# Optimization experiments

Hardware: AMD Instinct MI355X
Metric: run time of the kernel (lower is better)

## Reference

```python
import jax, jax.numpy as jnp
import numpy as np
import math

B, S, DIM = 1, 2048, 2048
H, KVH, HD = 32, 8, 64
REP = H // KVH


def _rope_cache(seqlen, head_dim, base=10000.0):
    # (seqlen, 2*head_dim): [cos | sin], each duplicated across both halves
    inv_freq = 1.0 / (base ** (np.arange(0, head_dim, 2, dtype=np.float32) / head_dim))
    t = np.arange(seqlen, dtype=np.float32)
    ang = np.outer(t, inv_freq)                    # (S, HD/2)
    ang = np.concatenate([ang, ang], axis=-1)      # (S, HD)
    return jnp.asarray(np.concatenate([np.cos(ang), np.sin(ang)], axis=-1))


def setup_inputs() -> dict:
    key = jax.random.key(0)
    ks = jax.random.split(key, 12)
    std = 0.02
    return {
        "x": jax.random.normal(ks[0], (B, S, DIM), jnp.float32),
        "rope_cache": _rope_cache(S, HD),
        "wq_w": jax.random.normal(ks[1], (H * HD, DIM), jnp.float32) * std,
        "wq_b": jax.random.normal(ks[2], (H * HD,), jnp.float32) * std,
        "wk_w": jax.random.normal(ks[3], (KVH * HD, DIM), jnp.float32) * std,
        "wk_b": jax.random.normal(ks[4], (KVH * HD,), jnp.float32) * std,
        "wv_w": jax.random.normal(ks[5], (KVH * HD, DIM), jnp.float32) * std,
        "wv_b": jax.random.normal(ks[6], (KVH * HD,), jnp.float32) * std,
        "wo_w": jax.random.normal(ks[7], (DIM, H * HD), jnp.float32) * std,
        "wo_b": jax.random.normal(ks[8], (DIM,), jnp.float32) * std,
        "sinks": jax.random.normal(ks[9], (H,), jnp.float32) * std,
    }


def _rotate_half(t):
    h = t.shape[-1] // 2
    return jnp.concatenate([-t[..., h:], t[..., :h]], axis=-1)


def reference(x, rope_cache, wq_w, wq_b, wk_w, wk_b, wv_w, wv_b, wo_w, wo_b, sinks):
    bsz, seqlen, _ = x.shape
    q = (jnp.einsum('bsd,od->bso', x, wq_w) + wq_b).reshape(bsz, seqlen, H, HD)
    k = (jnp.einsum('bsd,od->bso', x, wk_w) + wk_b).reshape(bsz, seqlen, KVH, HD)
    v = (jnp.einsum('bsd,od->bso', x, wv_w) + wv_b).reshape(bsz, seqlen, KVH, HD)

    cos = rope_cache[:seqlen, :HD][None, :, None, :]
    sin = rope_cache[:seqlen, HD:][None, :, None, :]
    q = q * cos + _rotate_half(q) * sin
    k = k * cos + _rotate_half(k) * sin

    # repeat_kv: repeat_interleave along head dim
    k = jnp.repeat(k, REP, axis=2)  # (B,S,H,HD)
    v = jnp.repeat(v, REP, axis=2)

    q = q.transpose(0, 2, 1, 3)  # (B,H,S,HD)
    k = k.transpose(0, 2, 1, 3)
    v = v.transpose(0, 2, 1, 3)

    scale = 1.0 / math.sqrt(HD)
    scores = jnp.einsum('bhqd,bhkd->bhqk', q, k) * scale
    causal = jnp.tril(jnp.ones((seqlen, seqlen), dtype=bool))
    scores = jnp.where(causal, scores, -jnp.inf)

    m = jnp.max(scores, axis=-1, keepdims=True)
    lse = m[..., 0] + jnp.log(jnp.sum(jnp.exp(scores - m), axis=-1))  # (B,H,S)
    attn = jnp.exp(scores - lse[..., None])
    out = jnp.einsum('bhqk,bhkd->bhqd', attn, v)

    # sink-token LSE renormalization
    combined_lse = jnp.logaddexp(lse, sinks[None, :, None])
    renorm = jnp.exp(jnp.clip(lse - combined_lse, -20.0, 0.0))
    out = out * renorm[..., None]

    out = out.transpose(0, 2, 1, 3).reshape(bsz, seqlen, H * HD)
    return jnp.einsum('bso,do->bsd', out, wo_w) + wo_b
```

## Files before the change

kernel.cpp:

```cpp
#include <hip/hip_runtime.h>


#define S_LEN 2048
#define DIM_  2048
#define QK_LD 2560

typedef __attribute__((ext_vector_type(8))) __bf16 bf16x8;
typedef __attribute__((ext_vector_type(4))) float f32x4;
typedef __attribute__((ext_vector_type(4))) unsigned short us4;

__device__ __forceinline__ unsigned short f2bf(float f) {
    union { float f; unsigned u; } v; v.f = f;
    unsigned r = v.u + 0x7FFFu + ((v.u >> 16) & 1u);
    return (unsigned short)(r >> 16);
}
__device__ __forceinline__ float bf2f(unsigned short u) {
    union { unsigned u; float f; } v; v.u = ((unsigned)u) << 16;
    return v.f;
}

__device__ __forceinline__ void gload_lds16(const void* g, void* l) {
    __builtin_amdgcn_global_load_lds(
        (const __attribute__((address_space(1))) void*)g,
        (__attribute__((address_space(3))) void*)l, 16, 0, 0);
}

__device__ __forceinline__ int swz32(int r, int ch) { return r*32 + ((ch ^ ((r >> 1) & 3)) << 3); }
__device__ __forceinline__ int swz64(int r, int ch) { return r*64 + ((ch ^ (r & 7)) << 3); }

__global__ void cvt_all(const float* __restrict__ x,  const float* __restrict__ wq,
                        const float* __restrict__ wk, const float* __restrict__ wv,
                        const float* __restrict__ wo,
                        unsigned short* __restrict__ xb,
                        unsigned short* __restrict__ wqkv,
                        unsigned short* __restrict__ wob) {
    const int i4 = blockIdx.x * 256 + threadIdx.x;
    const float* src; unsigned short* dst; int off;
    if (i4 < 1048576)      { src = x;  dst = xb;             off = i4; }
    else if (i4 < 2097152) { src = wq; dst = wqkv;           off = i4 - 1048576; }
    else if (i4 < 2359296) { src = wk; dst = wqkv + 4194304; off = i4 - 2097152; }
    else if (i4 < 2621440) { src = wv; dst = wqkv + 5242880; off = i4 - 2359296; }
    else                   { src = wo; dst = wob;            off = i4 - 2621440; }
    const float4 v = reinterpret_cast<const float4*>(src)[off];
    us4 o = { f2bf(v.x), f2bf(v.y), f2bf(v.z), f2bf(v.w) };
    reinterpret_cast<us4*>(dst)[off] = o;
}

__global__ void build_bias(const float* __restrict__ qb, const float* __restrict__ kb,
                           const float* __restrict__ vb, float* __restrict__ out) {
    const int i = blockIdx.x * 256 + threadIdx.x;
    if (i < 2048) out[i] = qb[i];
    else if (i < 2560) out[i] = kb[i - 2048];
    else if (i < 3072) out[i] = vb[i - 2560];
}

template<int MODE>
__global__ __launch_bounds__(256)
void gemm_bt(const unsigned short* __restrict__ A,
             const unsigned short* __restrict__ B,
             const float* __restrict__ bias,
             unsigned short* __restrict__ Cqk,
             unsigned short* __restrict__ Vt,
             float* __restrict__ Cf,
             int K)
{
    __shared__ unsigned short As[128 * 32];
    __shared__ unsigned short Bs[128 * 32];
    const int t = threadIdx.x;
    const int lane = t & 63;
    const int w = t >> 6;
    const int wr = w >> 1, wc = w & 1;
    const int lq = lane & 15;
    const int g = lane >> 4;
    const int m0 = blockIdx.y * 128;
    const int n0 = blockIdx.x * 128;

    const f32x4 z = {0.f, 0.f, 0.f, 0.f};
    f32x4 acc[4][4];
    #pragma unroll
    for (int i = 0; i < 4; i++)
        #pragma unroll
        for (int j = 0; j < 4; j++) acc[i][j] = z;

    for (int k0 = 0; k0 < K; k0 += 32) {
        #pragma unroll
        for (int c = 0; c < 2; c++) {
            const int chunk = w * 128 + c * 64 + lane;
            const int r = chunk >> 2;
            const int chl = (chunk & 3) ^ ((r >> 1) & 3);
            gload_lds16(&A[(size_t)(m0 + r) * K + k0 + (chl << 3)],
                        &As[(size_t)(w * 128 + c * 64) * 8]);
            gload_lds16(&B[(size_t)(n0 + r) * K + k0 + (chl << 3)],
                        &Bs[(size_t)(w * 128 + c * 64) * 8]);
        }
        __syncthreads();
        bf16x8 a[4], b[4];
        #pragma unroll
        for (int mi = 0; mi < 4; mi++)
            a[mi] = *reinterpret_cast<const bf16x8*>(&As[swz32(wr * 64 + mi * 16 + lq, g)]);
        #pragma unroll
        for (int ni = 0; ni < 4; ni++)
            b[ni] = *reinterpret_cast<const bf16x8*>(&Bs[swz32(wc * 64 + ni * 16 + lq, g)]);
        #pragma unroll
        for (int mi = 0; mi < 4; mi++)
            #pragma unroll
            for (int ni = 0; ni < 4; ni++)
                acc[mi][ni] = __builtin_amdgcn_mfma_f32_16x16x32_bf16(a[mi], b[ni], acc[mi][ni], 0, 0, 0);
        __syncthreads();
    }

    #pragma unroll
    for (int mi = 0; mi < 4; mi++) {
        const int row0 = m0 + wr * 64 + mi * 16 + g * 4;
        #pragma unroll
        for (int ni = 0; ni < 4; ni++) {
            const int col = n0 + wc * 64 + ni * 16 + lq;
            const float bv = bias[col];
            if (MODE == 1) {
                #pragma unroll
                for (int j = 0; j < 4; j++)
                    Cf[(size_t)(row0 + j) * 2048 + col] = acc[mi][ni][j] + bv;
            } else {
                if (col < 2560) {
                    const float qs = (col < 2048) ? 0.1803368801f : 1.0f;
                    #pragma unroll
                    for (int j = 0; j < 4; j++)
                        Cqk[(size_t)(row0 + j) * QK_LD + col] = f2bf((acc[mi][ni][j] + bv) * qs);
                } else {
                    us4 pk;
                    #pragma unroll
                    for (int j = 0; j < 4; j++) pk[j] = f2bf(acc[mi][ni][j] + bv);
                    *reinterpret_cast<us4*>(&Vt[(size_t)(col - 2560) * S_LEN + row0]) = pk;
                }
            }
        }
    }
}

__global__ void rope_kernel(unsigned short* __restrict__ qk, const float* __restrict__ rope) {
    const int idx = blockIdx.x * 256 + threadIdx.x;
    const int s = idx / 1280;
    const int rem = idx - s * 1280;
    const int head = rem >> 5;
    const int p = rem & 31;
    const size_t base = (size_t)s * QK_LD + head * 64 + p;
    const float c = rope[s * 128 + p];
    const float sn = rope[s * 128 + 64 + p];
    const float x0 = bf2f(qk[base]);
    const float x1 = bf2f(qk[base + 32]);
    qk[base]      = f2bf(x0 * c - x1 * sn);
    qk[base + 32] = f2bf(x1 * c + x0 * sn);
}

__global__ __launch_bounds__(256)
void attn_kernel(const unsigned short* __restrict__ qk,
                 const unsigned short* __restrict__ vt,
                 const float* __restrict__ sinks,
                 unsigned short* __restrict__ aout)
{
    const int pid = blockIdx.x;
    const int h = blockIdx.y;
    const int hkv = h >> 2;
    const int t = threadIdx.x;
    const int lane = t & 63;
    const int w = t >> 6;
    const int lq = lane & 15;
    const int g = lane >> 4;

    __shared__ unsigned short Ks[64 * 64];
    __shared__ unsigned short Vs[64 * 64];
    __shared__ unsigned short Ps[4][16 * 64];
    unsigned short* Pw = &Ps[w][0];

    const float sink = sinks[h];
    const f32x4 z = {0.f, 0.f, 0.f, 0.f};

    for (int pass = 0; pass < 2; ++pass) {
        const int qb = pass ? (31 - pid) : pid;
        const int qrow_a = qb * 64 + w * 16 + lq;
        const int qrow_c = qb * 64 + w * 16 + g * 4;

        bf16x8 aq[2];
        #pragma unroll
        for (int c = 0; c < 2; c++)
            aq[c] = *reinterpret_cast<const bf16x8*>(&qk[(size_t)qrow_a * QK_LD + h * 64 + c * 32 + g * 8]);

        f32x4 acc_o[4];
        #pragma unroll
        for (int df = 0; df < 4; df++) acc_o[df] = z;
        float mrow[4] = {-1e30f, -1e30f, -1e30f, -1e30f};
        float lrow[4] = {0.f, 0.f, 0.f, 0.f};

        bf16x8 kreg[2], vreg[2];
        #pragma unroll
        for (int i = 0; i < 2; i++) {
            const int e = i * 256 + t, r = e >> 3, ch = e & 7;
            kreg[i] = *reinterpret_cast<const bf16x8*>(&qk[(size_t)r * QK_LD + 2048 + hkv * 64 + (ch << 3)]);
            vreg[i] = *reinterpret_cast<const bf16x8*>(&vt[(size_t)(hkv * 64 + r) * S_LEN + (ch << 3)]);
        }

        for (int tkv = 0; tkv <= qb; tkv++) {
            __syncthreads();
            #pragma unroll
            for (int i = 0; i < 2; i++) {
                const int e = i * 256 + t, r = e >> 3, ch = e & 7;
                *reinterpret_cast<bf16x8*>(&Ks[swz64(r, ch)]) = kreg[i];
                *reinterpret_cast<bf16x8*>(&Vs[swz64(r, ch)]) = vreg[i];
            }
            __syncthreads();
            if (tkv < qb) {
                const int kvn = (tkv + 1) * 64;
                #pragma unroll
                for (int i = 0; i < 2; i++) {
                    const int e = i * 256 + t, r = e >> 3, ch = e & 7;
                    kreg[i] = *reinterpret_cast<const bf16x8*>(&qk[(size_t)(kvn + r) * QK_LD + 2048 + hkv * 64 + (ch << 3)]);
                    vreg[i] = *reinterpret_cast<const bf16x8*>(&vt[(size_t)(hkv * 64 + r) * S_LEN + kvn + (ch << 3)]);
                }
            }

            f32x4 sc[4];
            #pragma unroll
            for (int kf = 0; kf < 4; kf++) {
                sc[kf] = z;
                #pragma unroll
                for (int c = 0; c < 2; c++) {
                    const bf16x8 bk = *reinterpret_cast<const bf16x8*>(&Ks[swz64(kf * 16 + lq, c * 4 + g)]);
                    sc[kf] = __builtin_amdgcn_mfma_f32_16x16x32_bf16(aq[c], bk, sc[kf], 0, 0, 0);
                }
            }

            if (tkv == qb) {
                const int kv0 = tkv * 64;
                #pragma unroll
                for (int kf = 0; kf < 4; kf++) {
                    const int kvcol = kv0 + kf * 16 + lq;
                    #pragma unroll
                    for (int j = 0; j < 4; j++)
                        if (kvcol > qrow_c + j) sc[kf][j] = -1e30f;
                }
            }

            #pragma unroll
            for (int j = 0; j < 4; j++) {
                float mx = fmaxf(fmaxf(sc[0][j], sc[1][j]), fmaxf(sc[2][j], sc[3][j]));
                mx = fmaxf(mx, __shfl_xor(mx, 1));
                mx = fmaxf(mx, __shfl_xor(mx, 2));
                mx = fmaxf(mx, __shfl_xor(mx, 4));
                mx = fmaxf(mx, __shfl_xor(mx, 8));
                const float mnew = fmaxf(mrow[j], mx);
                const float resc = exp2f(mrow[j] - mnew);
                mrow[j] = mnew;
                float sum = 0.f;
                #pragma unroll
                for (int kf = 0; kf < 4; kf++) {
                    const float p = exp2f(sc[kf][j] - mnew);
                    sc[kf][j] = p;
                    sum += p;
                }
                sum += __shfl_xor(sum, 1);
                sum += __shfl_xor(sum, 2);
                sum += __shfl_xor(sum, 4);
                sum += __shfl_xor(sum, 8);
                lrow[j] = lrow[j] * resc + sum;
                #pragma unroll
                for (int df = 0; df < 4; df++) acc_o[df][j] *= resc;
            }

            #pragma unroll
            for (int kf = 0; kf < 4; kf++) {
                const int chb = kf * 2 + (lq >> 3);
                #pragma unroll
                for (int j = 0; j < 4; j++) {
                    const int prow = g * 4 + j;
                    Pw[prow * 64 + ((chb ^ (prow & 7)) << 3) + (lq & 7)] = f2bf(sc[kf][j]);
                }
            }
            #pragma unroll
            for (int c = 0; c < 2; c++) {
                const bf16x8 pa = *reinterpret_cast<const bf16x8*>(&Pw[lq * 64 + (((c * 4 + g) ^ (lq & 7)) << 3)]);
                #pragma unroll
                for (int df = 0; df < 4; df++) {
                    const bf16x8 bv = *reinterpret_cast<const bf16x8*>(&Vs[swz64(df * 16 + lq, c * 4 + g)]);
                    acc_o[df] = __builtin_amdgcn_mfma_f32_16x16x32_bf16(pa, bv, acc_o[df], 0, 0, 0);
                }
            }
        }

        #pragma unroll
        for (int j = 0; j < 4; j++) {
            const float lse = 0.6931471806f * (mrow[j] + log2f(lrow[j]));
            const float d = sink - lse;
            float f = (d > 20.f) ? d : log1pf(__expf(d));
            if (f > 20.f) f = 20.f;
            const float fac = __expf(-f) / lrow[j];
            const int row = qrow_c + j;
            #pragma unroll
            for (int df = 0; df < 4; df++)
                aout[(size_t)row * DIM_ + h * 64 + df * 16 + lq] = f2bf(acc_o[df][j] * fac);
        }
    }
}

extern "C" void kernel_launch(void* const* d_in, const int* in_sizes, int n_in,
                              void* d_out, int out_size, void* d_ws, size_t ws_size,
                              hipStream_t stream) {
    const float* x     = (const float*)d_in[0];
    const float* rope  = (const float*)d_in[1];
    const float* wq_w  = (const float*)d_in[2];
    const float* wq_b  = (const float*)d_in[3];
    const float* wk_w  = (const float*)d_in[4];
    const float* wk_b  = (const float*)d_in[5];
    const float* wv_w  = (const float*)d_in[6];
    const float* wv_b  = (const float*)d_in[7];
    const float* wo_w  = (const float*)d_in[8];
    const float* wo_b  = (const float*)d_in[9];
    const float* sinks = (const float*)d_in[10];
    float* out = (float*)d_out;

    char* ws = (char*)d_ws;
    unsigned short* xb    = (unsigned short*)(ws);
    unsigned short* wqkv  = (unsigned short*)(ws + (8u  << 20));
    unsigned short* wob   = (unsigned short*)(ws + (20u << 20));
    unsigned short* qkbuf = (unsigned short*)(ws + (28u << 20));
    unsigned short* vtbuf = (unsigned short*)(ws + (38u << 20));
    unsigned short* abuf  = (unsigned short*)(ws + (40u << 20));
    float*          bcat  = (float*)(ws + (48u << 20));

    cvt_all<<<14336, 256, 0, stream>>>(x, wq_w, wk_w, wv_w, wo_w, xb, wqkv, wob);
    build_bias<<<12, 256, 0, stream>>>(wq_b, wk_b, wv_b, bcat);

    gemm_bt<0><<<dim3(24, 16), 256, 0, stream>>>(xb, wqkv, bcat, qkbuf, vtbuf, nullptr, 2048);
    rope_kernel<<<10240, 256, 0, stream>>>(qkbuf, rope);
    attn_kernel<<<dim3(16, 32), 256, 0, stream>>>(qkbuf, vtbuf, sinks, abuf);
    gemm_bt<1><<<dim3(16, 16), 256, 0, stream>>>(abuf, wob, wo_b, nullptr, nullptr, out, 2048);
}
```

Before: 293.3 us.

## Double-buffer GEMM and attention LDS tiles, transpose attention MFMAs, one q-block per CTA

The GEMM now double-buffers its LDS tiles, so the next K slice loads while the current one is multiplied. This removes one barrier per iteration. The attention kernel drops the paired two-pass scheme and launches one CTA per query block, heaviest blocks first, with double-buffered K/V tiles. It also swaps the MFMA operand order so each lane holds one full query row, which shrinks the softmax reductions to two shuffles and allows vectorized P and output stores. The costs are more LDS per block and lost load balance from the paired causal blocks, offset by the reversed block ordering.

Result: no change. 288.0 us (-1.8%).

```diff
diff --git a/kernel.cpp b/kernel.cpp
--- a/kernel.cpp
+++ b/kernel.cpp
@@ -64,8 +64,8 @@
              float* __restrict__ Cf,
              int K)
 {
-    __shared__ unsigned short As[128 * 32];
-    __shared__ unsigned short Bs[128 * 32];
+    __shared__ unsigned short As[2][128 * 32];
+    __shared__ unsigned short Bs[2][128 * 32];
     const int t = threadIdx.x;
     const int lane = t & 63;
     const int w = t >> 6;
@@ -82,25 +82,32 @@
         #pragma unroll
         for (int j = 0; j < 4; j++) acc[i][j] = z;
 
-    for (int k0 = 0; k0 < K; k0 += 32) {
+    auto stage = [&](int buf, int k0) {
         #pragma unroll
         for (int c = 0; c < 2; c++) {
             const int chunk = w * 128 + c * 64 + lane;
             const int r = chunk >> 2;
             const int chl = (chunk & 3) ^ ((r >> 1) & 3);
             gload_lds16(&A[(size_t)(m0 + r) * K + k0 + (chl << 3)],
-                        &As[(size_t)(w * 128 + c * 64) * 8]);
+                        &As[buf][(size_t)(w * 128 + c * 64) * 8]);
             gload_lds16(&B[(size_t)(n0 + r) * K + k0 + (chl << 3)],
-                        &Bs[(size_t)(w * 128 + c * 64) * 8]);
-        }
-        __syncthreads();
+                        &Bs[buf][(size_t)(w * 128 + c * 64) * 8]);
+        }
+    };
+
+    stage(0, 0);
+    __syncthreads();
+    const int NIT = K >> 5;
+    for (int it = 0; it < NIT; ++it) {
+        const int cur = it & 1;
+        if (it + 1 < NIT) stage(cur ^ 1, (it + 1) << 5);
         bf16x8 a[4], b[4];
         #pragma unroll
         for (int mi = 0; mi < 4; mi++)
-            a[mi] = *reinterpret_cast<const bf16x8*>(&As[swz32(wr * 64 + mi * 16 + lq, g)]);
+            a[mi] = *reinterpret_cast<const bf16x8*>(&As[cur][swz32(wr * 64 + mi * 16 + lq, g)]);
         #pragma unroll
         for (int ni = 0; ni < 4; ni++)
-            b[ni] = *reinterpret_cast<const bf16x8*>(&Bs[swz32(wc * 64 + ni * 16 + lq, g)]);
+            b[ni] = *reinterpret_cast<const bf16x8*>(&Bs[cur][swz32(wc * 64 + ni * 16 + lq, g)]);
         #pragma unroll
         for (int mi = 0; mi < 4; mi++)
             #pragma unroll
@@ -158,8 +165,8 @@
                  const float* __restrict__ sinks,
                  unsigned short* __restrict__ aout)
 {
-    const int pid = blockIdx.x;
-    const int h = blockIdx.y;
+    const int qb  = 31 - blockIdx.x;
+    const int h   = blockIdx.y;
     const int hkv = h >> 2;
     const int t = threadIdx.x;
     const int lane = t & 63;
@@ -167,137 +174,135 @@
     const int lq = lane & 15;
     const int g = lane >> 4;
 
-    __shared__ unsigned short Ks[64 * 64];
-    __shared__ unsigned short Vs[64 * 64];
+    __shared__ unsigned short Ks[2][64 * 64];
+    __shared__ unsigned short Vs[2][64 * 64];
     __shared__ unsigned short Ps[4][16 * 64];
     unsigned short* Pw = &Ps[w][0];
 
-    const float sink = sinks[h];
+    const int qrow = qb * 64 + w * 16 + lq;
+
+    bf16x8 aq[2];
+    #pragma unroll
+    for (int c = 0; c < 2; c++)
+        aq[c] = *reinterpret_cast<const bf16x8*>(&qk[(size_t)qrow * QK_LD + h * 64 + c * 32 + g * 8]);
+
     const f32x4 z = {0.f, 0.f, 0.f, 0.f};
-
-    for (int pass = 0; pass < 2; ++pass) {
-        const int qb = pass ? (31 - pid) : pid;
-        const int qrow_a = qb * 64 + w * 16 + lq;
-        const int qrow_c = qb * 64 + w * 16 + g * 4;
-
-        bf16x8 aq[2];
-        #pragma unroll
-        for (int c = 0; c < 2; c++)
-            aq[c] = *reinterpret_cast<const bf16x8*>(&qk[(size_t)qrow_a * QK_LD + h * 64 + c * 32 + g * 8]);
-
-        f32x4 acc_o[4];
-        #pragma unroll
-        for (int df = 0; df < 4; df++) acc_o[df] = z;
-        float mrow[4] = {-1e30f, -1e30f, -1e30f, -1e30f};
-        float lrow[4] = {0.f, 0.f, 0.f, 0.f};
-
-        bf16x8 kreg[2], vreg[2];
-        #pragma unroll
-        for (int i = 0; i < 2; i++) {
-            const int e = i * 256 + t, r = e >> 3, ch = e & 7;
-            kreg[i] = *reinterpret_cast<const bf16x8*>(&qk[(size_t)r * QK_LD + 2048 + hkv * 64 + (ch << 3)]);
-            vreg[i] = *reinterpret_cast<const bf16x8*>(&vt[(size_t)(hkv * 64 + r) * S_LEN + (ch << 3)]);
-        }
-
-        for (int tkv = 0; tkv <= qb; tkv++) {
-            __syncthreads();
+    f32x4 acc[4];
+    #pragma unroll
+    for (int df = 0; df < 4; df++) acc[df] = z;
+    float m = -1e30f, l = 0.f;
+
+    bf16x8 kreg[2], vreg[2];
+    #pragma unroll
+    for (int i = 0; i < 2; i++) {
+        const int e = i * 256 + t, r = e >> 3, ch = e & 7;
+        kreg[i] = *reinterpret_cast<const bf16x8*>(&qk[(size_t)r * QK_LD + 2048 + hkv * 64 + (ch << 3)]);
+        vreg[i] = *reinterpret_cast<const bf16x8*>(&vt[(size_t)(hkv * 64 + r) * S_LEN + (ch << 3)]);
+    }
+    #pragma unroll
+    for (int i = 0; i < 2; i++) {
+        const int e = i * 256 + t, r = e >> 3, ch = e & 7;
+        *reinterpret_cast<bf16x8*>(&Ks[0][swz64(r, ch)]) = kreg[i];
+        *reinterpret_cast<bf16x8*>(&Vs[0][swz64(r, ch)]) = vreg[i];
+    }
+    __syncthreads();
+
+    for (int tkv = 0; tkv <= qb; tkv++) {
+        const int cur = tkv & 1;
+        if (tkv < qb) {
+            const int kvn = (tkv + 1) * 64;
             #pragma unroll
             for (int i = 0; i < 2; i++) {
                 const int e = i * 256 + t, r = e >> 3, ch = e & 7;
-                *reinterpret_cast<bf16x8*>(&Ks[swz64(r, ch)]) = kreg[i];
-                *reinterpret_cast<bf16x8*>(&Vs[swz64(r, ch)]) = vreg[i];
-            }
-            __syncthreads();
-            if (tkv < qb) {
-                const int kvn = (tkv + 1) * 64;
+                kreg[i] = *reinterpret_cast<const bf16x8*>(&qk[(size_t)(kvn + r) * QK_LD + 2048 + hkv * 64 + (ch << 3)]);
+                vreg[i] = *reinterpret_cast<const bf16x8*>(&vt[(size_t)(hkv * 64 + r) * S_LEN + kvn + (ch << 3)]);
+            }
+        }
+
+        f32x4 sc[4];
+        #pragma unroll
+        for (int f = 0; f < 4; f++) {
+            sc[f] = z;
+            #pragma unroll
+            for (int c = 0; c < 2; c++) {
+                const bf16x8 bk = *reinterpret_cast<const bf16x8*>(&Ks[cur][swz64(f * 16 + lq, c * 4 + g)]);
+                sc[f] = __builtin_amdgcn_mfma_f32_16x16x32_bf16(bk, aq[c], sc[f], 0, 0, 0);
+            }
+        }
+
+        if (tkv == qb) {
+            const int thr = w * 16 + lq - g * 4;
+            #pragma unroll
+            for (int f = 0; f < 4; f++)
                 #pragma unroll
-                for (int i = 0; i < 2; i++) {
-                    const int e = i * 256 + t, r = e >> 3, ch = e & 7;
-                    kreg[i] = *reinterpret_cast<const bf16x8*>(&qk[(size_t)(kvn + r) * QK_LD + 2048 + hkv * 64 + (ch << 3)]);
-                    vreg[i] = *reinterpret_cast<const bf16x8*>(&vt[(size_t)(hkv * 64 + r) * S_LEN + kvn + (ch << 3)]);
-                }
-            }
-
-            f32x4 sc[4];
-            #pragma unroll
-            for (int kf = 0; kf < 4; kf++) {
-                sc[kf] = z;
-                #pragma unroll
-                for (int c = 0; c < 2; c++) {
-                    const bf16x8 bk = *reinterpret_cast<const bf16x8*>(&Ks[swz64(kf * 16 + lq, c * 4 + g)]);
-                    sc[kf] = __builtin_amdgcn_mfma_f32_16x16x32_bf16(aq[c], bk, sc[kf], 0, 0, 0);
-                }
-            }
-
-            if (tkv == qb) {
-                const int kv0 = tkv * 64;
-                #pragma unroll
-                for (int kf = 0; kf < 4; kf++) {
-                    const int kvcol = kv0 + kf * 16 + lq;
-                    #pragma unroll
-                    for (int j = 0; j < 4; j++)
-                        if (kvcol > qrow_c + j) sc[kf][j] = -1e30f;
-                }
-            }
-
+                for (int j = 0; j < 4; j++)
+                    if (f * 16 + j > thr) sc[f][j] = -1e30f;
+        }
+
+        float mx = sc[0][0];
+        #pragma unroll
+        for (int f = 0; f < 4; f++)
+            #pragma unroll
+            for (int j = 0; j < 4; j++) mx = fmaxf(mx, sc[f][j]);
+        mx = fmaxf(mx, __shfl_xor(mx, 16));
+        mx = fmaxf(mx, __shfl_xor(mx, 32));
+        const float mn = fmaxf(m, mx);
+        const float rs = exp2f(m - mn);
+        m = mn;
+        float s = 0.f;
+        #pragma unroll
+        for (int f = 0; f < 4; f++)
             #pragma unroll
             for (int j = 0; j < 4; j++) {
-                float mx = fmaxf(fmaxf(sc[0][j], sc[1][j]), fmaxf(sc[2][j], sc[3][j]));
-                mx = fmaxf(mx, __shfl_xor(mx, 1));
-                mx = fmaxf(mx, __shfl_xor(mx, 2));
-                mx = fmaxf(mx, __shfl_xor(mx, 4));
-                mx = fmaxf(mx, __shfl_xor(mx, 8));
-                const float mnew = fmaxf(mrow[j], mx);
-                const float resc = exp2f(mrow[j] - mnew);
-                mrow[j] = mnew;
-                float sum = 0.f;
-                #pragma unroll
-                for (int kf = 0; kf < 4; kf++) {
-                    const float p = exp2f(sc[kf][j] - mnew);
-                    sc[kf][j] = p;
-                    sum += p;
-                }
-                sum += __shfl_xor(sum, 1);
-                sum += __shfl_xor(sum, 2);
-                sum += __shfl_xor(sum, 4);
-                sum += __shfl_xor(sum, 8);
-                lrow[j] = lrow[j] * resc + sum;
-                #pragma unroll
-                for (int df = 0; df < 4; df++) acc_o[df][j] *= resc;
-            }
-
-            #pragma unroll
-            for (int kf = 0; kf < 4; kf++) {
-                const int chb = kf * 2 + (lq >> 3);
-                #pragma unroll
-                for (int j = 0; j < 4; j++) {
-                    const int prow = g * 4 + j;
-                    Pw[prow * 64 + ((chb ^ (prow & 7)) << 3) + (lq & 7)] = f2bf(sc[kf][j]);
-                }
-            }
-            #pragma unroll
-            for (int c = 0; c < 2; c++) {
-                const bf16x8 pa = *reinterpret_cast<const bf16x8*>(&Pw[lq * 64 + (((c * 4 + g) ^ (lq & 7)) << 3)]);
-                #pragma unroll
-                for (int df = 0; df < 4; df++) {
-                    const bf16x8 bv = *reinterpret_cast<const bf16x8*>(&Vs[swz64(df * 16 + lq, c * 4 + g)]);
-                    acc_o[df] = __builtin_amdgcn_mfma_f32_16x16x32_bf16(pa, bv, acc_o[df], 0, 0, 0);
-                }
-            }
-        }
-
-        #pragma unroll
-        for (int j = 0; j < 4; j++) {
-            const float lse = 0.6931471806f * (mrow[j] + log2f(lrow[j]));
-            const float d = sink - lse;
-            float f = (d > 20.f) ? d : log1pf(__expf(d));
-            if (f > 20.f) f = 20.f;
-            const float fac = __expf(-f) / lrow[j];
-            const int row = qrow_c + j;
-            #pragma unroll
-            for (int df = 0; df < 4; df++)
-                aout[(size_t)row * DIM_ + h * 64 + df * 16 + lq] = f2bf(acc_o[df][j] * fac);
-        }
+                const float p = exp2f(sc[f][j] - mn);
+                sc[f][j] = p;
+                s += p;
+            }
+        s += __shfl_xor(s, 16);
+        s += __shfl_xor(s, 32);
+        l = l * rs + s;
+        #pragma unroll
+        for (int df = 0; df < 4; df++) acc[df] *= rs;
+
+        #pragma unroll
+        for (int f = 0; f < 4; f++) {
+            us4 pk = { f2bf(sc[f][0]), f2bf(sc[f][1]), f2bf(sc[f][2]), f2bf(sc[f][3]) };
+            *reinterpret_cast<us4*>(
+                &Pw[lq * 64 + ((((f << 1) | (g >> 1)) ^ (lq & 7)) << 3) + ((g & 1) << 2)]) = pk;
+        }
+        #pragma unroll
+        for (int c = 0; c < 2; c++) {
+            const bf16x8 pb = *reinterpret_cast<const bf16x8*>(
+                &Pw[lq * 64 + (((c * 4 + g) ^ (lq & 7)) << 3)]);
+            #pragma unroll
+            for (int df = 0; df < 4; df++) {
+                const bf16x8 bv = *reinterpret_cast<const bf16x8*>(&Vs[cur][swz64(df * 16 + lq, c * 4 + g)]);
+                acc[df] = __builtin_amdgcn_mfma_f32_16x16x32_bf16(bv, pb, acc[df], 0, 0, 0);
+            }
+        }
+
+        if (tkv < qb) {
+            #pragma unroll
+            for (int i = 0; i < 2; i++) {
+                const int e = i * 256 + t, r = e >> 3, ch = e & 7;
+                *reinterpret_cast<bf16x8*>(&Ks[cur ^ 1][swz64(r, ch)]) = kreg[i];
+                *reinterpret_cast<bf16x8*>(&Vs[cur ^ 1][swz64(r, ch)]) = vreg[i];
+            }
+        }
+        __syncthreads();
+    }
+
+    const float sink = sinks[h];
+    const float lse = 0.6931471806f * (m + log2f(l));
+    const float d = sink - lse;
+    float f = (d > 20.f) ? d : log1pf(__expf(d));
+    if (f > 20.f) f = 20.f;
+    const float fac = __expf(-f) / l;
+    #pragma unroll
+    for (int df = 0; df < 4; df++) {
+        us4 pk = { f2bf(acc[df][0] * fac), f2bf(acc[df][1] * fac),
+                   f2bf(acc[df][2] * fac), f2bf(acc[df][3] * fac) };
+        *reinterpret_cast<us4*>(&aout[(size_t)qrow * DIM_ + h * 64 + df * 16 + g * 4]) = pk;
     }
 }
 
@@ -331,6 +336,6 @@
 
     gemm_bt<0><<<dim3(24, 16), 256, 0, stream>>>(xb, wqkv, bcat, qkbuf, vtbuf, nullptr, 2048);
     rope_kernel<<<10240, 256, 0, stream>>>(qkbuf, rope);
-    attn_kernel<<<dim3(16, 32), 256, 0, stream>>>(qkbuf, vtbuf, sinks, abuf);
+    attn_kernel<<<dim3(32, 32), 256, 0, stream>>>(qkbuf, vtbuf, sinks, abuf);
     gemm_bt<1><<<dim3(16, 16), 256, 0, stream>>>(abuf, wob, wo_b, nullptr, nullptr, out, 2048);
 }
```
